# Kernel optimization log

Hardware: AMD Instinct MI355X
Metric: run time of the kernel (lower is better)

## Reference

```python
import jax, jax.numpy as jnp
import numpy as np

N_NODES = 1_000_000
N_EDGES = 26_000_000


def setup_inputs() -> dict:
    key = jax.random.key(0)
    ks = jax.random.split(key, 10)
    x = jax.random.normal(ks[0], (N_NODES, 3), dtype=jnp.float32)
    edge_index = jax.random.randint(ks[1], (2, N_EDGES), 0, N_NODES, dtype=jnp.int64)
    edge_attr = jax.random.normal(ks[2], (N_EDGES, 1), dtype=jnp.float32)
    u = jax.random.normal(ks[3], (1, 8), dtype=jnp.float32)
    batch = jnp.zeros((N_NODES,), dtype=jnp.int64)
    # node_mlp params: Lin(6,16) -> ReLU -> Lin(16,16) -> ReLU -> Lin(16,3)
    s1 = 1.0 / np.sqrt(6.0)
    s2 = 1.0 / np.sqrt(16.0)
    W1 = jax.random.uniform(ks[4], (6, 16), minval=-s1, maxval=s1, dtype=jnp.float32)
    b1 = jax.random.uniform(ks[5], (16,), minval=-s1, maxval=s1, dtype=jnp.float32)
    W2 = jax.random.uniform(ks[6], (16, 16), minval=-s2, maxval=s2, dtype=jnp.float32)
    b2 = jax.random.uniform(ks[7], (16,), minval=-s2, maxval=s2, dtype=jnp.float32)
    W3 = jax.random.uniform(ks[8], (16, 3), minval=-s2, maxval=s2, dtype=jnp.float32)
    b3 = jax.random.uniform(ks[9], (3,), minval=-s2, maxval=s2, dtype=jnp.float32)
    return {"x": x, "edge_index": edge_index, "edge_attr": edge_attr, "u": u,
            "batch": batch, "W1": W1, "b1": b1, "W2": W2, "b2": b2, "W3": W3, "b3": b3}


def reference(x, edge_index, edge_attr, u, batch, W1, b1, W2, b2, W3, b3):
    row, col = edge_index[0], edge_index[1]
    # gather source-node features along edges, scatter-sum into target nodes
    agg = jax.ops.segment_sum(x[row], col, num_segments=x.shape[0])  # [N, 3]
    h = jnp.concatenate([x, agg], axis=1)  # [N, 6]
    h = jax.nn.relu(h @ W1 + b1)
    h = jax.nn.relu(h @ W2 + b2)
    return h @ W3 + b3  # [N, 3]
```

## Files before the change

### kernel.cpp

```cpp
#include <hip/hip_runtime.h>


#define SHIFT 12
#define BSIZE 4096
#define MAXNB 1024
#define NBLK  512
#define AGG_THREADS 1024


__global__ __launch_bounds__(256) void hist_kernel(
    const int* __restrict__ cols, int* __restrict__ hist,
    int nb, int chunk, int n_edges)
{
    __shared__ int lh[MAXNB];
    const int t = threadIdx.x, b = blockIdx.x;
    for (int k = t; k < nb; k += 256) lh[k] = 0;
    __syncthreads();

    long long s = (long long)b * chunk;
    long long e = s + chunk; if (e > n_edges) e = n_edges;
    if (s < e) {
        const int n = (int)(e - s);
        const int n4 = n >> 2;
        const int4* __restrict__ c4p = reinterpret_cast<const int4*>(cols + s);
        for (int i = t; i < n4; i += 256) {
            int4 c = c4p[i];
            atomicAdd(&lh[(unsigned)c.x >> SHIFT], 1);
            atomicAdd(&lh[(unsigned)c.y >> SHIFT], 1);
            atomicAdd(&lh[(unsigned)c.z >> SHIFT], 1);
            atomicAdd(&lh[(unsigned)c.w >> SHIFT], 1);
        }
        for (int i = (n4 << 2) + t; i < n; i += 256)
            atomicAdd(&lh[(unsigned)cols[s + i] >> SHIFT], 1);
    }
    __syncthreads();
    for (int k = t; k < nb; k += 256) hist[(size_t)b * nb + k] = lh[k];
}

__global__ __launch_bounds__(NBLK) void scan_blocks_kernel(
    int* __restrict__ hist, int* __restrict__ colTotal, int nb)
{
    __shared__ int sd[NBLK];
    const int t = threadIdx.x, k = blockIdx.x;
    const int v = hist[(size_t)t * nb + k];
    sd[t] = v; __syncthreads();
#pragma unroll
    for (int off = 1; off < NBLK; off <<= 1) {
        int a = (t >= off) ? sd[t - off] : 0;
        __syncthreads();
        sd[t] += a;
        __syncthreads();
    }
    hist[(size_t)t * nb + k] = sd[t] - v;
    if (t == NBLK - 1) colTotal[k] = sd[t];
}

__global__ __launch_bounds__(MAXNB) void scan_buckets_kernel(
    const int* __restrict__ colTotal, int* __restrict__ bucketStart, int nb)
{
    __shared__ int sd[MAXNB];
    const int t = threadIdx.x;
    const int v = (t < nb) ? colTotal[t] : 0;
    sd[t] = v; __syncthreads();
#pragma unroll
    for (int off = 1; off < MAXNB; off <<= 1) {
        int a = (t >= off) ? sd[t - off] : 0;
        __syncthreads();
        sd[t] += a;
        __syncthreads();
    }
    if (t < nb) bucketStart[t] = sd[t] - v;
    if (t == 0) bucketStart[nb] = sd[MAXNB - 1];
}

__global__ __launch_bounds__(256) void scatter_kernel(
    const int* __restrict__ rows, const int* __restrict__ cols,
    const int* __restrict__ hist, const int* __restrict__ bucketStart,
    unsigned* __restrict__ packed, int nb, int chunk, int n_edges)
{
    __shared__ int lc[MAXNB];
    const int t = threadIdx.x, b = blockIdx.x;
    for (int k = t; k < nb; k += 256)
        lc[k] = bucketStart[k] + hist[(size_t)b * nb + k];
    __syncthreads();

    long long s = (long long)b * chunk;
    long long e = s + chunk; if (e > n_edges) e = n_edges;
    if (s < e) {
        const int n = (int)(e - s);
        const int n4 = n >> 2;
        const int4* __restrict__ c4p = reinterpret_cast<const int4*>(cols + s);
        const int4* __restrict__ r4p = reinterpret_cast<const int4*>(rows + s);
        for (int i = t; i < n4; i += 256) {
            int4 c = c4p[i];
            int4 r = r4p[i];
            int p;
            p = atomicAdd(&lc[(unsigned)c.x >> SHIFT], 1);
            packed[p] = ((unsigned)r.x << SHIFT) | ((unsigned)c.x & (BSIZE - 1));
            p = atomicAdd(&lc[(unsigned)c.y >> SHIFT], 1);
            packed[p] = ((unsigned)r.y << SHIFT) | ((unsigned)c.y & (BSIZE - 1));
            p = atomicAdd(&lc[(unsigned)c.z >> SHIFT], 1);
            packed[p] = ((unsigned)r.z << SHIFT) | ((unsigned)c.z & (BSIZE - 1));
            p = atomicAdd(&lc[(unsigned)c.w >> SHIFT], 1);
            packed[p] = ((unsigned)r.w << SHIFT) | ((unsigned)c.w & (BSIZE - 1));
        }
        for (int i = (n4 << 2) + t; i < n; i += 256) {
            int c = cols[s + i], r = rows[s + i];
            int p = atomicAdd(&lc[(unsigned)c >> SHIFT], 1);
            packed[p] = ((unsigned)r << SHIFT) | ((unsigned)c & (BSIZE - 1));
        }
    }
}

__global__ __launch_bounds__(AGG_THREADS) void bucket_agg_kernel(
    const unsigned* __restrict__ packed, const float* __restrict__ x,
    const int* __restrict__ bucketStart, float* __restrict__ out,
    int n_nodes)
{
    __shared__ float acc[BSIZE * 3];
    const int t = threadIdx.x, k = blockIdx.x;
    for (int f = t; f < BSIZE * 3; f += AGG_THREADS) acc[f] = 0.0f;
    __syncthreads();

    const int s = bucketStart[k];
    const int e = bucketStart[k + 1];

    int i = s + t;
    for (; i + 3 * AGG_THREADS < e; i += 4 * AGG_THREADS) {
        unsigned p0 = packed[i];
        unsigned p1 = packed[i + AGG_THREADS];
        unsigned p2 = packed[i + 2 * AGG_THREADS];
        unsigned p3 = packed[i + 3 * AGG_THREADS];
        const float* xs0 = x + 3ll * (p0 >> SHIFT);
        const float* xs1 = x + 3ll * (p1 >> SHIFT);
        const float* xs2 = x + 3ll * (p2 >> SHIFT);
        const float* xs3 = x + 3ll * (p3 >> SHIFT);
        float a0 = xs0[0], b0 = xs0[1], c0 = xs0[2];
        float a1 = xs1[0], b1 = xs1[1], c1 = xs1[2];
        float a2 = xs2[0], b2 = xs2[1], c2 = xs2[2];
        float a3 = xs3[0], b3 = xs3[1], c3 = xs3[2];
        int j0 = (int)(p0 & (BSIZE - 1)) * 3;
        int j1 = (int)(p1 & (BSIZE - 1)) * 3;
        int j2 = (int)(p2 & (BSIZE - 1)) * 3;
        int j3 = (int)(p3 & (BSIZE - 1)) * 3;
        atomicAdd(&acc[j0 + 0], a0); atomicAdd(&acc[j0 + 1], b0); atomicAdd(&acc[j0 + 2], c0);
        atomicAdd(&acc[j1 + 0], a1); atomicAdd(&acc[j1 + 1], b1); atomicAdd(&acc[j1 + 2], c1);
        atomicAdd(&acc[j2 + 0], a2); atomicAdd(&acc[j2 + 1], b2); atomicAdd(&acc[j2 + 2], c2);
        atomicAdd(&acc[j3 + 0], a3); atomicAdd(&acc[j3 + 1], b3); atomicAdd(&acc[j3 + 2], c3);
    }
    for (; i < e; i += AGG_THREADS) {
        const unsigned p = packed[i];
        const float* __restrict__ xs = x + 3ll * (p >> SHIFT);
        const int j = (int)(p & (BSIZE - 1)) * 3;
        atomicAdd(&acc[j + 0], xs[0]);
        atomicAdd(&acc[j + 1], xs[1]);
        atomicAdd(&acc[j + 2], xs[2]);
    }
    __syncthreads();

    const long long base = (long long)k << SHIFT;
    long long lim = (long long)n_nodes - base;
    if (lim > BSIZE) lim = BSIZE;
    if (lim <= 0) return;
    float* __restrict__ o = out + base * 3;
    const int fl = (int)lim * 3;
    for (int f = t; f < fl; f += AGG_THREADS) o[f] = acc[f];
}


__global__ __launch_bounds__(256) void edge_scatter_kernel(
    const int* __restrict__ rows, const int* __restrict__ cols,
    const float* __restrict__ x, float* __restrict__ agg, int n_edges)
{
    const long long tid = (long long)blockIdx.x * blockDim.x + threadIdx.x;
    const long long stride = (long long)gridDim.x * blockDim.x;
    for (long long i = tid; i < n_edges; i += stride) {
        int r = rows[i], c = cols[i];
        const float* xs = x + 3ll * r; float* a = agg + 3ll * c;
        atomicAdd(a + 0, xs[0]); atomicAdd(a + 1, xs[1]); atomicAdd(a + 2, xs[2]);
    }
}


__global__ __launch_bounds__(256) void node_mlp_kernel(
    const float* __restrict__ x,
    const float* __restrict__ W1, const float* __restrict__ b1,
    const float* __restrict__ W2, const float* __restrict__ b2,
    const float* __restrict__ W3, const float* __restrict__ b3,
    float* __restrict__ out, int n_nodes)
{
    __shared__ float sW1[96];
    __shared__ float sb1[16];
    __shared__ float sW2[256];
    __shared__ float sb2[16];
    __shared__ float sW3[48];
    __shared__ float sb3[3];

    const int t = threadIdx.x;
    if (t < 96)  sW1[t] = W1[t];
    if (t < 16)  sb1[t] = b1[t];
    sW2[t] = W2[t];
    if (t < 16)  sb2[t] = b2[t];
    if (t < 48)  sW3[t] = W3[t];
    if (t < 3)   sb3[t] = b3[t];
    __syncthreads();

    const int i = blockIdx.x * 256 + t;
    if (i >= n_nodes) return;

    float in6[6];
    in6[0] = x[3 * i + 0];
    in6[1] = x[3 * i + 1];
    in6[2] = x[3 * i + 2];
    in6[3] = out[3 * i + 0];
    in6[4] = out[3 * i + 1];
    in6[5] = out[3 * i + 2];

    float h1[16];
#pragma unroll
    for (int j = 0; j < 16; ++j) {
        float s = sb1[j];
#pragma unroll
        for (int k = 0; k < 6; ++k) s = fmaf(in6[k], sW1[k * 16 + j], s);
        h1[j] = fmaxf(s, 0.0f);
    }

    float h2[16];
#pragma unroll
    for (int j = 0; j < 16; ++j) {
        float s = sb2[j];
#pragma unroll
        for (int k = 0; k < 16; ++k) s = fmaf(h1[k], sW2[k * 16 + j], s);
        h2[j] = fmaxf(s, 0.0f);
    }

    float o[3];
#pragma unroll
    for (int c = 0; c < 3; ++c) {
        float s = sb3[c];
#pragma unroll
        for (int j = 0; j < 16; ++j) s = fmaf(h2[j], sW3[j * 3 + c], s);
        o[c] = s;
    }

    out[3 * i + 0] = o[0];
    out[3 * i + 1] = o[1];
    out[3 * i + 2] = o[2];
}

extern "C" void kernel_launch(void* const* d_in, const int* in_sizes, int n_in,
                              void* d_out, int out_size, void* d_ws, size_t ws_size,
                              hipStream_t stream) {
    const float* x   = (const float*)d_in[0];
    const int*   ei  = (const int*)d_in[1];
    const float* W1  = (const float*)d_in[5];
    const float* b1  = (const float*)d_in[6];
    const float* W2  = (const float*)d_in[7];
    const float* b2  = (const float*)d_in[8];
    const float* W3  = (const float*)d_in[9];
    const float* b3  = (const float*)d_in[10];

    const int n_nodes = in_sizes[0] / 3;
    const int n_edges = in_sizes[1] / 2;
    const int* rows = ei;
    const int* cols = ei + n_edges;
    float* out = (float*)d_out;

    const int nb = (n_nodes + BSIZE - 1) >> SHIFT;

    const size_t need = (size_t)n_edges * 4 + (size_t)NBLK * nb * 4
                      + (size_t)nb * 4 + (size_t)(nb + 1) * 4;
    const bool fast = (ws_size >= need) && (nb <= MAXNB)
                   && (n_nodes <= (1 << (32 - SHIFT)));

    if (fast) {
        unsigned* packed    = (unsigned*)d_ws;
        int* hist           = (int*)(packed + n_edges);
        int* colTotal       = hist + (size_t)NBLK * nb;
        int* bucketStart    = colTotal + nb;

        int chunk = (n_edges + NBLK - 1) / NBLK;
        chunk = (chunk + 3) & ~3;

        hist_kernel<<<NBLK, 256, 0, stream>>>(cols, hist, nb, chunk, n_edges);
        scan_blocks_kernel<<<nb, NBLK, 0, stream>>>(hist, colTotal, nb);
        scan_buckets_kernel<<<1, MAXNB, 0, stream>>>(colTotal, bucketStart, nb);
        scatter_kernel<<<NBLK, 256, 0, stream>>>(rows, cols, hist, bucketStart,
                                                 packed, nb, chunk, n_edges);
        bucket_agg_kernel<<<nb, AGG_THREADS, 0, stream>>>(packed, x, bucketStart, out, n_nodes);
    } else {
        hipMemsetAsync(d_out, 0, (size_t)out_size * sizeof(float), stream);
        edge_scatter_kernel<<<8192, 256, 0, stream>>>(rows, cols, x, out, n_edges);
    }

    const int nblocks = (n_nodes + 255) / 256;
    node_mlp_kernel<<<nblocks, 256, 0, stream>>>(x, W1, b1, W2, b2, W3, b3, out, n_nodes);
}
```

Baseline: 728.2 us.

## Sub-sort edges by source-row range within column buckets and fuse node MLP into aggregation

```diff
diff --git a/kernel.cpp b/kernel.cpp
--- a/kernel.cpp
+++ b/kernel.cpp
@@ -1,20 +1,21 @@
 #include <hip/hip_runtime.h>
 
 
-#define SHIFT 12
-#define BSIZE 4096
-#define MAXNB 1024
-#define NBLK  512
+#define CSHIFT 12
+#define BSIZE  4096
+#define RSHIFT 17
+#define MAXKEYS 4096
+#define NBLK   128
 #define AGG_THREADS 1024
 
 
 __global__ __launch_bounds__(256) void hist_kernel(
-    const int* __restrict__ cols, int* __restrict__ hist,
-    int nb, int chunk, int n_edges)
-{
-    __shared__ int lh[MAXNB];
+    const int* __restrict__ rows, const int* __restrict__ cols,
+    int* __restrict__ hist, int nkeys, int G, int chunk, int n_edges)
+{
+    __shared__ int lh[MAXKEYS];
     const int t = threadIdx.x, b = blockIdx.x;
-    for (int k = t; k < nb; k += 256) lh[k] = 0;
+    for (int k = t; k < nkeys; k += 256) lh[k] = 0;
     __syncthreads();
 
     long long s = (long long)b * chunk;
@@ -23,26 +24,30 @@
         const int n = (int)(e - s);
         const int n4 = n >> 2;
         const int4* __restrict__ c4p = reinterpret_cast<const int4*>(cols + s);
+        const int4* __restrict__ r4p = reinterpret_cast<const int4*>(rows + s);
         for (int i = t; i < n4; i += 256) {
             int4 c = c4p[i];
-            atomicAdd(&lh[(unsigned)c.x >> SHIFT], 1);
-            atomicAdd(&lh[(unsigned)c.y >> SHIFT], 1);
-            atomicAdd(&lh[(unsigned)c.z >> SHIFT], 1);
-            atomicAdd(&lh[(unsigned)c.w >> SHIFT], 1);
-        }
-        for (int i = (n4 << 2) + t; i < n; i += 256)
-            atomicAdd(&lh[(unsigned)cols[s + i] >> SHIFT], 1);
-    }
-    __syncthreads();
-    for (int k = t; k < nb; k += 256) hist[(size_t)b * nb + k] = lh[k];
+            int4 r = r4p[i];
+            atomicAdd(&lh[((unsigned)c.x >> CSHIFT) * G + ((unsigned)r.x >> RSHIFT)], 1);
+            atomicAdd(&lh[((unsigned)c.y >> CSHIFT) * G + ((unsigned)r.y >> RSHIFT)], 1);
+            atomicAdd(&lh[((unsigned)c.z >> CSHIFT) * G + ((unsigned)r.z >> RSHIFT)], 1);
+            atomicAdd(&lh[((unsigned)c.w >> CSHIFT) * G + ((unsigned)r.w >> RSHIFT)], 1);
+        }
+        for (int i = (n4 << 2) + t; i < n; i += 256) {
+            int c = cols[s + i], r = rows[s + i];
+            atomicAdd(&lh[((unsigned)c >> CSHIFT) * G + ((unsigned)r >> RSHIFT)], 1);
+        }
+    }
+    __syncthreads();
+    for (int k = t; k < nkeys; k += 256) hist[(size_t)b * nkeys + k] = lh[k];
 }
 
 __global__ __launch_bounds__(NBLK) void scan_blocks_kernel(
-    int* __restrict__ hist, int* __restrict__ colTotal, int nb)
+    int* __restrict__ hist, int* __restrict__ keyTotal, int nkeys)
 {
     __shared__ int sd[NBLK];
     const int t = threadIdx.x, k = blockIdx.x;
-    const int v = hist[(size_t)t * nb + k];
+    const int v = hist[(size_t)t * nkeys + k];
     sd[t] = v; __syncthreads();
 #pragma unroll
     for (int off = 1; off < NBLK; off <<= 1) {
@@ -51,37 +56,41 @@
         sd[t] += a;
         __syncthreads();
     }
-    hist[(size_t)t * nb + k] = sd[t] - v;
-    if (t == NBLK - 1) colTotal[k] = sd[t];
-}
-
-__global__ __launch_bounds__(MAXNB) void scan_buckets_kernel(
-    const int* __restrict__ colTotal, int* __restrict__ bucketStart, int nb)
-{
-    __shared__ int sd[MAXNB];
+    hist[(size_t)t * nkeys + k] = sd[t] - v;
+    if (t == NBLK - 1) keyTotal[k] = sd[t];
+}
+
+__global__ __launch_bounds__(1024) void scan_keys_kernel(
+    const int* __restrict__ keyTotal, int* __restrict__ keyStart, int nkeys)
+{
+    __shared__ int sd[1024];
     const int t = threadIdx.x;
-    const int v = (t < nb) ? colTotal[t] : 0;
-    sd[t] = v; __syncthreads();
-#pragma unroll
-    for (int off = 1; off < MAXNB; off <<= 1) {
+    const int i0 = 2 * t, i1 = 2 * t + 1;
+    const int v0 = (i0 < nkeys) ? keyTotal[i0] : 0;
+    const int v1 = (i1 < nkeys) ? keyTotal[i1] : 0;
+    sd[t] = v0 + v1; __syncthreads();
+#pragma unroll
+    for (int off = 1; off < 1024; off <<= 1) {
         int a = (t >= off) ? sd[t - off] : 0;
         __syncthreads();
         sd[t] += a;
         __syncthreads();
     }
-    if (t < nb) bucketStart[t] = sd[t] - v;
-    if (t == 0) bucketStart[nb] = sd[MAXNB - 1];
+    const int base = sd[t] - (v0 + v1);
+    if (i0 < nkeys) keyStart[i0] = base;
+    if (i1 < nkeys) keyStart[i1] = base + v0;
+    if (t == 1023) keyStart[nkeys] = sd[1023];
 }
 
 __global__ __launch_bounds__(256) void scatter_kernel(
     const int* __restrict__ rows, const int* __restrict__ cols,
-    const int* __restrict__ hist, const int* __restrict__ bucketStart,
-    unsigned* __restrict__ packed, int nb, int chunk, int n_edges)
-{
-    __shared__ int lc[MAXNB];
+    const int* __restrict__ hist, const int* __restrict__ keyStart,
+    unsigned* __restrict__ packed, int nkeys, int G, int chunk, int n_edges)
+{
+    __shared__ int lc[MAXKEYS];
     const int t = threadIdx.x, b = blockIdx.x;
-    for (int k = t; k < nb; k += 256)
-        lc[k] = bucketStart[k] + hist[(size_t)b * nb + k];
+    for (int k = t; k < nkeys; k += 256)
+        lc[k] = keyStart[k] + hist[(size_t)b * nkeys + k];
     __syncthreads();
 
     long long s = (long long)b * chunk;
@@ -95,35 +104,46 @@
             int4 c = c4p[i];
             int4 r = r4p[i];
             int p;
-            p = atomicAdd(&lc[(unsigned)c.x >> SHIFT], 1);
-            packed[p] = ((unsigned)r.x << SHIFT) | ((unsigned)c.x & (BSIZE - 1));
-            p = atomicAdd(&lc[(unsigned)c.y >> SHIFT], 1);
-            packed[p] = ((unsigned)r.y << SHIFT) | ((unsigned)c.y & (BSIZE - 1));
-            p = atomicAdd(&lc[(unsigned)c.z >> SHIFT], 1);
-            packed[p] = ((unsigned)r.z << SHIFT) | ((unsigned)c.z & (BSIZE - 1));
-            p = atomicAdd(&lc[(unsigned)c.w >> SHIFT], 1);
-            packed[p] = ((unsigned)r.w << SHIFT) | ((unsigned)c.w & (BSIZE - 1));
+            p = atomicAdd(&lc[((unsigned)c.x >> CSHIFT) * G + ((unsigned)r.x >> RSHIFT)], 1);
+            packed[p] = ((unsigned)r.x << CSHIFT) | ((unsigned)c.x & (BSIZE - 1));
+            p = atomicAdd(&lc[((unsigned)c.y >> CSHIFT) * G + ((unsigned)r.y >> RSHIFT)], 1);
+            packed[p] = ((unsigned)r.y << CSHIFT) | ((unsigned)c.y & (BSIZE - 1));
+            p = atomicAdd(&lc[((unsigned)c.z >> CSHIFT) * G + ((unsigned)r.z >> RSHIFT)], 1);
+            packed[p] = ((unsigned)r.z << CSHIFT) | ((unsigned)c.z & (BSIZE - 1));
+            p = atomicAdd(&lc[((unsigned)c.w >> CSHIFT) * G + ((unsigned)r.w >> RSHIFT)], 1);
+            packed[p] = ((unsigned)r.w << CSHIFT) | ((unsigned)c.w & (BSIZE - 1));
         }
         for (int i = (n4 << 2) + t; i < n; i += 256) {
             int c = cols[s + i], r = rows[s + i];
-            int p = atomicAdd(&lc[(unsigned)c >> SHIFT], 1);
-            packed[p] = ((unsigned)r << SHIFT) | ((unsigned)c & (BSIZE - 1));
-        }
-    }
-}
-
-__global__ __launch_bounds__(AGG_THREADS) void bucket_agg_kernel(
+            int p = atomicAdd(&lc[((unsigned)c >> CSHIFT) * G + ((unsigned)r >> RSHIFT)], 1);
+            packed[p] = ((unsigned)r << CSHIFT) | ((unsigned)c & (BSIZE - 1));
+        }
+    }
+}
+
+__global__ __launch_bounds__(AGG_THREADS) void bucket_agg_mlp_kernel(
     const unsigned* __restrict__ packed, const float* __restrict__ x,
-    const int* __restrict__ bucketStart, float* __restrict__ out,
-    int n_nodes)
+    const int* __restrict__ keyStart,
+    const float* __restrict__ W1, const float* __restrict__ b1,
+    const float* __restrict__ W2, const float* __restrict__ b2,
+    const float* __restrict__ W3, const float* __restrict__ b3,
+    float* __restrict__ out, int n_nodes, int G)
 {
     __shared__ float acc[BSIZE * 3];
+    __shared__ float sW1[96], sb1[16], sW2[256], sb2[16], sW3[48], sb3[3];
     const int t = threadIdx.x, k = blockIdx.x;
+
+    if (t < 96)  sW1[t] = W1[t];
+    if (t < 16)  sb1[t] = b1[t];
+    if (t < 256) sW2[t] = W2[t];
+    if (t >= 256 && t < 272) sb2[t - 256] = b2[t - 256];
+    if (t >= 272 && t < 320) sW3[t - 272] = W3[t - 272];
+    if (t >= 320 && t < 323) sb3[t - 320] = b3[t - 320];
     for (int f = t; f < BSIZE * 3; f += AGG_THREADS) acc[f] = 0.0f;
     __syncthreads();
 
-    const int s = bucketStart[k];
-    const int e = bucketStart[k + 1];
+    const int s = keyStart[k * G];
+    const int e = keyStart[k * G + G];
 
     int i = s + t;
     for (; i + 3 * AGG_THREADS < e; i += 4 * AGG_THREADS) {
@@ -131,26 +151,26 @@
         unsigned p1 = packed[i + AGG_THREADS];
         unsigned p2 = packed[i + 2 * AGG_THREADS];
         unsigned p3 = packed[i + 3 * AGG_THREADS];
-        const float* xs0 = x + 3ll * (p0 >> SHIFT);
-        const float* xs1 = x + 3ll * (p1 >> SHIFT);
-        const float* xs2 = x + 3ll * (p2 >> SHIFT);
-        const float* xs3 = x + 3ll * (p3 >> SHIFT);
+        const float* xs0 = x + 3ll * (p0 >> CSHIFT);
+        const float* xs1 = x + 3ll * (p1 >> CSHIFT);
+        const float* xs2 = x + 3ll * (p2 >> CSHIFT);
+        const float* xs3 = x + 3ll * (p3 >> CSHIFT);
         float a0 = xs0[0], b0 = xs0[1], c0 = xs0[2];
-        float a1 = xs1[0], b1 = xs1[1], c1 = xs1[2];
-        float a2 = xs2[0], b2 = xs2[1], c2 = xs2[2];
-        float a3 = xs3[0], b3 = xs3[1], c3 = xs3[2];
+        float a1 = xs1[0], b1v = xs1[1], c1 = xs1[2];
+        float a2 = xs2[0], b2v = xs2[1], c2 = xs2[2];
+        float a3 = xs3[0], b3v = xs3[1], c3 = xs3[2];
         int j0 = (int)(p0 & (BSIZE - 1)) * 3;
         int j1 = (int)(p1 & (BSIZE - 1)) * 3;
         int j2 = (int)(p2 & (BSIZE - 1)) * 3;
         int j3 = (int)(p3 & (BSIZE - 1)) * 3;
-        atomicAdd(&acc[j0 + 0], a0); atomicAdd(&acc[j0 + 1], b0); atomicAdd(&acc[j0 + 2], c0);
-        atomicAdd(&acc[j1 + 0], a1); atomicAdd(&acc[j1 + 1], b1); atomicAdd(&acc[j1 + 2], c1);
-        atomicAdd(&acc[j2 + 0], a2); atomicAdd(&acc[j2 + 1], b2); atomicAdd(&acc[j2 + 2], c2);
-        atomicAdd(&acc[j3 + 0], a3); atomicAdd(&acc[j3 + 1], b3); atomicAdd(&acc[j3 + 2], c3);
+        atomicAdd(&acc[j0 + 0], a0); atomicAdd(&acc[j0 + 1], b0);  atomicAdd(&acc[j0 + 2], c0);
+        atomicAdd(&acc[j1 + 0], a1); atomicAdd(&acc[j1 + 1], b1v); atomicAdd(&acc[j1 + 2], c1);
+        atomicAdd(&acc[j2 + 0], a2); atomicAdd(&acc[j2 + 1], b2v); atomicAdd(&acc[j2 + 2], c2);
+        atomicAdd(&acc[j3 + 0], a3); atomicAdd(&acc[j3 + 1], b3v); atomicAdd(&acc[j3 + 2], c3);
     }
     for (; i < e; i += AGG_THREADS) {
         const unsigned p = packed[i];
-        const float* __restrict__ xs = x + 3ll * (p >> SHIFT);
+        const float* __restrict__ xs = x + 3ll * (p >> CSHIFT);
         const int j = (int)(p & (BSIZE - 1)) * 3;
         atomicAdd(&acc[j + 0], xs[0]);
         atomicAdd(&acc[j + 1], xs[1]);
@@ -158,13 +178,48 @@
     }
     __syncthreads();
 
-    const long long base = (long long)k << SHIFT;
+    const long long base = (long long)k << CSHIFT;
     long long lim = (long long)n_nodes - base;
     if (lim > BSIZE) lim = BSIZE;
     if (lim <= 0) return;
-    float* __restrict__ o = out + base * 3;
-    const int fl = (int)lim * 3;
-    for (int f = t; f < fl; f += AGG_THREADS) o[f] = acc[f];
+
+    for (int j = t; j < (int)lim; j += AGG_THREADS) {
+        const long long node = base + j;
+        float in6[6];
+        in6[0] = x[3 * node + 0];
+        in6[1] = x[3 * node + 1];
+        in6[2] = x[3 * node + 2];
+        in6[3] = acc[3 * j + 0];
+        in6[4] = acc[3 * j + 1];
+        in6[5] = acc[3 * j + 2];
+
+        float h1[16];
+#pragma unroll
+        for (int q = 0; q < 16; ++q) {
+            float sv = sb1[q];
+#pragma unroll
+            for (int r = 0; r < 6; ++r) sv = fmaf(in6[r], sW1[r * 16 + q], sv);
+            h1[q] = fmaxf(sv, 0.0f);
+        }
+        float h2[16];
+#pragma unroll
+        for (int q = 0; q < 16; ++q) {
+            float sv = sb2[q];
+#pragma unroll
+            for (int r = 0; r < 16; ++r) sv = fmaf(h1[r], sW2[r * 16 + q], sv);
+            h2[q] = fmaxf(sv, 0.0f);
+        }
+        float o0 = sb3[0], o1 = sb3[1], o2 = sb3[2];
+#pragma unroll
+        for (int q = 0; q < 16; ++q) {
+            o0 = fmaf(h2[q], sW3[q * 3 + 0], o0);
+            o1 = fmaf(h2[q], sW3[q * 3 + 1], o1);
+            o2 = fmaf(h2[q], sW3[q * 3 + 2], o2);
+        }
+        out[3 * node + 0] = o0;
+        out[3 * node + 1] = o1;
+        out[3 * node + 2] = o2;
+    }
 }
 
 
@@ -181,7 +236,6 @@
     }
 }
 
-
 __global__ __launch_bounds__(256) void node_mlp_kernel(
     const float* __restrict__ x,
     const float* __restrict__ W1, const float* __restrict__ b1,
@@ -189,13 +243,7 @@
     const float* __restrict__ W3, const float* __restrict__ b3,
     float* __restrict__ out, int n_nodes)
 {
-    __shared__ float sW1[96];
-    __shared__ float sb1[16];
-    __shared__ float sW2[256];
-    __shared__ float sb2[16];
-    __shared__ float sW3[48];
-    __shared__ float sb3[3];
-
+    __shared__ float sW1[96], sb1[16], sW2[256], sb2[16], sW3[48], sb3[3];
     const int t = threadIdx.x;
     if (t < 96)  sW1[t] = W1[t];
     if (t < 16)  sb1[t] = b1[t];
@@ -224,7 +272,6 @@
         for (int k = 0; k < 6; ++k) s = fmaf(in6[k], sW1[k * 16 + j], s);
         h1[j] = fmaxf(s, 0.0f);
     }
-
     float h2[16];
 #pragma unroll
     for (int j = 0; j < 16; ++j) {
@@ -233,7 +280,6 @@
         for (int k = 0; k < 16; ++k) s = fmaf(h1[k], sW2[k * 16 + j], s);
         h2[j] = fmaxf(s, 0.0f);
     }
-
     float o[3];
 #pragma unroll
     for (int c = 0; c < 3; ++c) {
@@ -242,7 +288,6 @@
         for (int j = 0; j < 16; ++j) s = fmaf(h2[j], sW3[j * 3 + c], s);
         o[c] = s;
     }
-
     out[3 * i + 0] = o[0];
     out[3 * i + 1] = o[1];
     out[3 * i + 2] = o[2];
@@ -266,33 +311,35 @@
     const int* cols = ei + n_edges;
     float* out = (float*)d_out;
 
-    const int nb = (n_nodes + BSIZE - 1) >> SHIFT;
-
-    const size_t need = (size_t)n_edges * 4 + (size_t)NBLK * nb * 4
-                      + (size_t)nb * 4 + (size_t)(nb + 1) * 4;
-    const bool fast = (ws_size >= need) && (nb <= MAXNB)
-                   && (n_nodes <= (1 << (32 - SHIFT)));
+    const int nb = (n_nodes + BSIZE - 1) >> CSHIFT;
+    const int G  = (n_nodes + (1 << RSHIFT) - 1) >> RSHIFT;
+    const int nkeys = nb * G;
+
+    const size_t need = (size_t)n_edges * 4 + (size_t)NBLK * nkeys * 4
+                      + (size_t)nkeys * 4 + (size_t)(nkeys + 1) * 4;
+    const bool fast = (ws_size >= need) && (nkeys <= MAXKEYS) && (nkeys <= 2048)
+                   && (n_nodes <= (1 << 20));
 
     if (fast) {
-        unsigned* packed    = (unsigned*)d_ws;
-        int* hist           = (int*)(packed + n_edges);
-        int* colTotal       = hist + (size_t)NBLK * nb;
-        int* bucketStart    = colTotal + nb;
+        unsigned* packed = (unsigned*)d_ws;
+        int* hist        = (int*)(packed + n_edges);
+        int* keyTotal    = hist + (size_t)NBLK * nkeys;
+        int* keyStart    = keyTotal + nkeys;
 
         int chunk = (n_edges + NBLK - 1) / NBLK;
         chunk = (chunk + 3) & ~3;
 
-        hist_kernel<<<NBLK, 256, 0, stream>>>(cols, hist, nb, chunk, n_edges);
-        scan_blocks_kernel<<<nb, NBLK, 0, stream>>>(hist, colTotal, nb);
-        scan_buckets_kernel<<<1, MAXNB, 0, stream>>>(colTotal, bucketStart, nb);
-        scatter_kernel<<<NBLK, 256, 0, stream>>>(rows, cols, hist, bucketStart,
-                                                 packed, nb, chunk, n_edges);
-        bucket_agg_kernel<<<nb, AGG_THREADS, 0, stream>>>(packed, x, bucketStart, out, n_nodes);
+        hist_kernel<<<NBLK, 256, 0, stream>>>(rows, cols, hist, nkeys, G, chunk, n_edges);
+        scan_blocks_kernel<<<nkeys, NBLK, 0, stream>>>(hist, keyTotal, nkeys);
+        scan_keys_kernel<<<1, 1024, 0, stream>>>(keyTotal, keyStart, nkeys);
+        scatter_kernel<<<NBLK, 256, 0, stream>>>(rows, cols, hist, keyStart,
+                                                 packed, nkeys, G, chunk, n_edges);
+        bucket_agg_mlp_kernel<<<nb, AGG_THREADS, 0, stream>>>(
+            packed, x, keyStart, W1, b1, W2, b2, W3, b3, out, n_nodes, G);
     } else {
         hipMemsetAsync(d_out, 0, (size_t)out_size * sizeof(float), stream);
         edge_scatter_kernel<<<8192, 256, 0, stream>>>(rows, cols, x, out, n_edges);
-    }
-
-    const int nblocks = (n_nodes + 255) / 256;
-    node_mlp_kernel<<<nblocks, 256, 0, stream>>>(x, W1, b1, W2, b2, W3, b3, out, n_nodes);
-}
+        const int nblocks = (n_nodes + 255) / 256;
+        node_mlp_kernel<<<nblocks, 256, 0, stream>>>(x, W1, b1, W2, b2, W3, b3, out, n_nodes);
+    }
+}
```

Measured after the change: 1.450 ms. 1.99x slower.
